# Optimization experiments

Hardware: AMD Instinct MI355X
Metric: run time of the kernel (lower is better)

The kernel has to match this reference:

```python
import jax, jax.numpy as jnp
import numpy as np

D_MODEL = 1024
HEADS = 16
D_K = D_MODEL // HEADS


def setup_inputs() -> dict:
    key = jax.random.key(0)
    ks = jax.random.split(key, 12)
    B, S = 2, 2048
    scale = 1.0 / np.sqrt(D_MODEL)
    inp = {
        "q": jax.random.normal(ks[0], (B, S, D_MODEL), dtype=jnp.float32),
        "k": jax.random.normal(ks[1], (B, S, D_MODEL), dtype=jnp.float32),
        "v": jax.random.normal(ks[2], (B, S, D_MODEL), dtype=jnp.float32),
        "src_mask": jax.random.randint(ks[3], (B, 1, S), 0, 2, dtype=jnp.int32),
        # projection params (nn.Linear: y = x @ W.T + b); store W already transposed
        "Wq": jax.random.normal(ks[4], (D_MODEL, D_MODEL), dtype=jnp.float32) * scale,
        "bq": jnp.zeros((D_MODEL,), dtype=jnp.float32),
        "Wk": jax.random.normal(ks[5], (D_MODEL, D_MODEL), dtype=jnp.float32) * scale,
        "bk": jnp.zeros((D_MODEL,), dtype=jnp.float32),
        "Wv": jax.random.normal(ks[6], (D_MODEL, D_MODEL), dtype=jnp.float32) * scale,
        "bv": jnp.zeros((D_MODEL,), dtype=jnp.float32),
        "Wo": jax.random.normal(ks[7], (D_MODEL, D_MODEL), dtype=jnp.float32) * scale,
        "bo": jnp.zeros((D_MODEL,), dtype=jnp.float32),
    }
    return inp


def reference(q, k, v, src_mask, Wq, bq, Wk, bk, Wv, bv, Wo, bo):
    B, S, _ = q.shape
    # QKV projections, reshape to (b, heads, seq, d_k)
    def proj(x, W, b):
        y = x @ W + b  # (b, s, d_model)
        return y.reshape(B, S, HEADS, D_K).transpose(0, 2, 1, 3)

    qh = proj(q, Wq, bq)
    kh = proj(k, Wk, bk)
    vh = proj(v, Wv, bv)

    # scaled dot-product attention with padding mask
    scores = jnp.einsum("bhqd,bhkd->bhqk", qh, kh) / jnp.sqrt(jnp.float32(D_K))
    mask = src_mask[:, None, :, :]  # (b,1,1,s), broadcast over heads & query
    scores = jnp.where(mask == 0, jnp.float32(-1e9), scores)
    probs = jax.nn.softmax(scores, axis=-1)
    # dropout is identity in eval mode (reference baseline)
    ctx = jnp.einsum("bhqk,bhkd->bhqd", probs, vh)
    ctx = ctx.transpose(0, 2, 1, 3).reshape(B, S, D_MODEL)
    return ctx @ Wo + bo
```

## Files before the change

### kernel.cpp

```cpp
#include <hip/hip_runtime.h>
#include <hip/hip_bf16.h>

#define DM 1024
#define SL 2048
#define NH 16
#define DK 64

typedef __bf16 bf16;
typedef __bf16 bf16x8 __attribute__((ext_vector_type(8)));
typedef __bf16 bf16x4 __attribute__((ext_vector_type(4)));
typedef float f32x4 __attribute__((ext_vector_type(4)));
typedef float f32x16 __attribute__((ext_vector_type(16)));
typedef unsigned u32x4 __attribute__((ext_vector_type(4)));

__device__ __forceinline__ void gll16(const void* g, void* l) {
  __builtin_amdgcn_global_load_lds(
      (const __attribute__((address_space(1))) unsigned int*)g,
      (__attribute__((address_space(3))) unsigned int*)l, 16, 0, 0);
}

__device__ __forceinline__ unsigned pk2(float a, float b) {
  unsigned short lo = __builtin_bit_cast(unsigned short, (bf16)a);
  unsigned short hi = __builtin_bit_cast(unsigned short, (bf16)b);
  return (unsigned)lo | ((unsigned)hi << 16);
}

__global__ __launch_bounds__(256) void cvt_x_kernel(
    const float* __restrict__ q, const float* __restrict__ k, const float* __restrict__ v,
    bf16* __restrict__ xq, bf16* __restrict__ xk, bf16* __restrict__ xv) {
  const float* src; bf16* dst;
  if (blockIdx.y == 0)      { src = q; dst = xq; }
  else if (blockIdx.y == 1) { src = k; dst = xk; }
  else                      { src = v; dst = xv; }
  int i = (blockIdx.x * 256 + threadIdx.x) * 8;
  f32x4 a = *(const f32x4*)(src + i);
  f32x4 b = *(const f32x4*)(src + i + 4);
  bf16x8 o;
  o[0]=(bf16)a[0]; o[1]=(bf16)a[1]; o[2]=(bf16)a[2]; o[3]=(bf16)a[3];
  o[4]=(bf16)b[0]; o[5]=(bf16)b[1]; o[6]=(bf16)b[2]; o[7]=(bf16)b[3];
  *(bf16x8*)(dst + i) = o;
}

__global__ __launch_bounds__(256) void cvt_w_kernel(
    const float* __restrict__ W0, const float* __restrict__ W1,
    const float* __restrict__ W2, const float* __restrict__ W3,
    bf16* __restrict__ T0, bf16* __restrict__ T1,
    bf16* __restrict__ T2, bf16* __restrict__ T3) {
  const float* W; bf16* T;
  switch (blockIdx.y) {
    case 0:  W = W0; T = T0; break;
    case 1:  W = W1; T = T1; break;
    case 2:  W = W2; T = T2; break;
    default: W = W3; T = T3; break;
  }
  __shared__ float t[64][65];
  const int tid = threadIdx.x;
  const int tx = blockIdx.x & 15, ty = blockIdx.x >> 4;
  const int cr = tid >> 4, cc = tid & 15;
  #pragma unroll
  for (int rr = 0; rr < 4; ++rr) {
    int row = rr*16 + cr;
    f32x4 val = *(const f32x4*)(W + (ty*64 + row)*DM + tx*64 + cc*4);
    t[row][cc*4+0] = val[0]; t[row][cc*4+1] = val[1];
    t[row][cc*4+2] = val[2]; t[row][cc*4+3] = val[3];
  }
  __syncthreads();
  #pragma unroll
  for (int rr = 0; rr < 4; ++rr) {
    int nrow = rr*16 + cr;
    bf16x4 o;
    o[0] = (bf16)t[cc*4+0][nrow]; o[1] = (bf16)t[cc*4+1][nrow];
    o[2] = (bf16)t[cc*4+2][nrow]; o[3] = (bf16)t[cc*4+3][nrow];
    *(bf16x4*)(T + (tx*64 + nrow)*DM + ty*64 + cc*4) = o;
  }
}

__global__ __launch_bounds__(256) void maskcvt_kernel(
    const int* __restrict__ msk, float* __restrict__ mBias) {
  int i = (blockIdx.x * 256 + threadIdx.x) * 4;
  int4 m4 = *(const int4*)(msk + i);
  f32x4 o;
  o[0] = (m4.x == 0) ? -1.4426950e9f : 0.f;
  o[1] = (m4.y == 0) ? -1.4426950e9f : 0.f;
  o[2] = (m4.z == 0) ? -1.4426950e9f : 0.f;
  o[3] = (m4.w == 0) ? -1.4426950e9f : 0.f;
  *(f32x4*)(mBias + i) = o;
}

template<int MODE>
__device__ __forceinline__ void gemm_core(
    const bf16* __restrict__ A, const bf16* __restrict__ Bt, const float* __restrict__ bias,
    bf16* __restrict__ outH, float* __restrict__ outF) {
  const int bid = blockIdx.x;
  const int swz = (bid & 7) * 64 + (bid >> 3);
  const int mt = swz >> 3, nt = swz & 7;
  const int m0 = mt*64, n0 = nt*128;
  __shared__ __attribute__((aligned(16))) bf16 As[64*64];
  __shared__ __attribute__((aligned(16))) bf16 Bs[128*64];
  const int tid = threadIdx.x, lane = tid & 63, w = tid >> 6;
  const int wm = w >> 1, wn = w & 1;
  f32x4 acc[2][4];
  #pragma unroll
  for (int x = 0; x < 2; ++x)
    #pragma unroll
    for (int y = 0; y < 4; ++y)
      #pragma unroll
      for (int e = 0; e < 4; ++e) acc[x][y][e] = 0.f;

  for (int kt = 0; kt < 16; ++kt) {
    const int k0 = kt*64;
    __syncthreads();
    #pragma unroll
    for (int i = 0; i < 2; ++i) {
      int idx = (i*4 + w)*64 + lane;
      int r = idx >> 3;
      int s = (idx & 7) ^ (r & 7);
      gll16(A + (m0 + r)*DM + k0 + s*8, &As[(i*4 + w)*512]);
    }
    #pragma unroll
    for (int i = 0; i < 4; ++i) {
      int idx = (i*4 + w)*64 + lane;
      int r = idx >> 3;
      int s = (idx & 7) ^ (r & 7);
      gll16(Bt + (n0 + r)*DM + k0 + s*8, &Bs[(i*4 + w)*512]);
    }
    __syncthreads();
    bf16x8 bfr[4][2];
    #pragma unroll
    for (int ni = 0; ni < 4; ++ni) {
      int row = wn*64 + ni*16 + (lane & 15);
      #pragma unroll
      for (int c = 0; c < 2; ++c) {
        int slot = (lane >> 4) + c*4;
        bfr[ni][c] = *(const bf16x8*)&Bs[row*64 + ((slot ^ (row & 7)) << 3)];
      }
    }
    __builtin_amdgcn_s_setprio(1);
    #pragma unroll
    for (int mi = 0; mi < 2; ++mi) {
      int row = wm*32 + mi*16 + (lane & 15);
      bf16x8 a0 = *(const bf16x8*)&As[row*64 + ((((lane >> 4)    ) ^ (row & 7)) << 3)];
      bf16x8 a1 = *(const bf16x8*)&As[row*64 + ((((lane >> 4) + 4) ^ (row & 7)) << 3)];
      #pragma unroll
      for (int ni = 0; ni < 4; ++ni) {
        acc[mi][ni] = __builtin_amdgcn_mfma_f32_16x16x32_bf16(a0, bfr[ni][0], acc[mi][ni], 0, 0, 0);
        acc[mi][ni] = __builtin_amdgcn_mfma_f32_16x16x32_bf16(a1, bfr[ni][1], acc[mi][ni], 0, 0, 0);
      }
    }
    __builtin_amdgcn_s_setprio(0);
  }
  #pragma unroll
  for (int ni = 0; ni < 4; ++ni) {
    int n = n0 + wn*64 + ni*16 + (lane & 15);
    float bv = bias[n];
    #pragma unroll
    for (int mi = 0; mi < 2; ++mi) {
      int mb = m0 + wm*32 + mi*16 + ((lane >> 4) << 2);
      if (MODE == 2) {
        int bb = mb >> 11, ss = mb & 2047, hh = n >> 6, dd = n & 63;
        bf16x4 o;
        #pragma unroll
        for (int j = 0; j < 4; ++j) o[j] = (bf16)(acc[mi][ni][j] + bv);
        *(bf16x4*)&outH[(((bb << 4) + hh)*DK + dd)*SL + ss] = o;
      } else {
        #pragma unroll
        for (int j = 0; j < 4; ++j) {
          int m = mb + j;
          float val = acc[mi][ni][j] + bv;
          if (MODE == 1) {
            int bb = m >> 11, ss = m & 2047, hh = n >> 6, dd = n & 63;
            outH[(((bb << 4) + hh)*SL + ss)*DK + dd] = (bf16)val;
          } else {
            outF[m*DM + n] = val;
          }
        }
      }
    }
  }
}

__global__ __launch_bounds__(256, 4) void proj_gemm_kernel(
    const bf16* XQ, const bf16* XK, const bf16* XV,
    const bf16* WTQp, const bf16* WTKp, const bf16* WTVp,
    const float* bq, const float* bk, const float* bv,
    bf16* QHp, bf16* KHp, bf16* VTp) {
  if (blockIdx.y == 0)      gemm_core<1>(XQ, WTQp, bq, QHp, nullptr);
  else if (blockIdx.y == 1) gemm_core<1>(XK, WTKp, bk, KHp, nullptr);
  else                      gemm_core<2>(XV, WTVp, bv, VTp, nullptr);
}

__global__ __launch_bounds__(256, 4) void out_gemm_kernel(
    const bf16* CTXp, const bf16* WTOp, const float* bo, float* out) {
  gemm_core<0>(CTXp, WTOp, bo, nullptr, out);
}

__global__ __launch_bounds__(256, 2) void attn_kernel(
    const bf16* __restrict__ QHp, const bf16* __restrict__ KHp,
    const bf16* __restrict__ VTp, const float* __restrict__ mBias,
    bf16* __restrict__ CTXp) {
  const int d = blockIdx.x;
  const int xcd = d & 7, rr = d >> 3;
  const int bh = xcd*4 + (rr >> 4);
  const int qt = rr & 15;
  const int b = bh >> 4, h = bh & 15;
  const int q0 = qt * 128;
  const bf16* Qp  = QHp + bh * SL * DK;
  const bf16* Kp  = KHp + bh * SL * DK;
  const bf16* Vtp = VTp + bh * SL * DK;
  const float* mb_ = mBias + b * SL;
  __shared__ __attribute__((aligned(16))) bf16 Ks[2][64*64];
  __shared__ __attribute__((aligned(16))) bf16 Vts[2][64*64];
  const int tid = threadIdx.x, lane = tid & 63, w = tid >> 6;
  const int hi = lane >> 5, l5 = lane & 31;
  const float SCL2E = 0.18033688f;

  bf16x8 qf[4];
  {
    const bf16* qr = Qp + (q0 + w*32 + l5)*DK + hi*8;
    #pragma unroll
    for (int c = 0; c < 4; ++c) qf[c] = *(const bf16x8*)(qr + c*16);
  }
  f32x16 o0, o1;
  #pragma unroll
  for (int e = 0; e < 16; ++e) { o0[e] = 0.f; o1[e] = 0.f; }
  float m_run = -1e30f, l_run = 0.f;

  #define STAGE(buf, kt_)                                                  \
    {                                                                      \
      const int k0s = (kt_)*64;                                            \
      _Pragma("unroll")                                                    \
      for (int i = 0; i < 2; ++i) {                                        \
        int idx = (i*4 + w)*64 + lane;                                     \
        int r = idx >> 3;                                                  \
        int s = (idx & 7) ^ (r & 7);                                       \
        gll16(Kp + (k0s + r)*DK + s*8, &Ks[buf][(i*4 + w)*512]);           \
      }                                                                    \
      _Pragma("unroll")                                                    \
      for (int i = 0; i < 2; ++i) {                                        \
        int idx = (i*4 + w)*64 + lane;                                     \
        int r = idx >> 3;                                                  \
        int s = (idx & 7) ^ (r & 7);                                       \
        gll16(Vtp + r*SL + k0s + s*8, &Vts[buf][(i*4 + w)*512]);           \
      }                                                                    \
    }

  STAGE(0, 0);
  __syncthreads();

  for (int kt = 0; kt < 32; ++kt) {
    const int cur = kt & 1;
    const int k0 = kt*64;

    f32x4 mreg[2][4];
    #pragma unroll
    for (int half = 0; half < 2; ++half)
      #pragma unroll
      for (int qd = 0; qd < 4; ++qd)
        mreg[half][qd] = *(const f32x4*)&mb_[k0 + half*32 + qd*8 + hi*4];

    if (kt < 31) STAGE(cur ^ 1, kt + 1);

    f32x16 s0, s1;
    #pragma unroll
    for (int e = 0; e < 16; ++e) { s0[e] = 0.f; s1[e] = 0.f; }
    __builtin_amdgcn_s_setprio(1);
    #pragma unroll
    for (int c = 0; c < 4; ++c) {
      int sl = 2*c + hi;
      int r0 = l5, r1 = 32 + l5;
      bf16x8 kf0 = *(const bf16x8*)&Ks[cur][r0*64 + ((sl ^ (r0 & 7)) << 3)];
      bf16x8 kf1 = *(const bf16x8*)&Ks[cur][r1*64 + ((sl ^ (r1 & 7)) << 3)];
      s0 = __builtin_amdgcn_mfma_f32_32x32x16_bf16(kf0, qf[c], s0, 0, 0, 0);
      s1 = __builtin_amdgcn_mfma_f32_32x32x16_bf16(kf1, qf[c], s1, 0, 0, 0);
    }
    __builtin_amdgcn_s_setprio(0);

    float pv_[32];
    float mtv0 = -1e30f, mtv1 = -1e30f, mtv2 = -1e30f, mtv3 = -1e30f;
    #pragma unroll
    for (int half = 0; half < 2; ++half) {
      #pragma unroll
      for (int qd = 0; qd < 4; ++qd) {
        f32x4 ma = mreg[half][qd];
        #pragma unroll
        for (int j = 0; j < 4; ++j) {
          float val = (half ? s1[qd*4+j] : s0[qd*4+j]) * SCL2E + ma[j];
          pv_[half*16 + qd*4 + j] = val;
          if (j == 0) mtv0 = fmaxf(mtv0, val);
          else if (j == 1) mtv1 = fmaxf(mtv1, val);
          else if (j == 2) mtv2 = fmaxf(mtv2, val);
          else mtv3 = fmaxf(mtv3, val);
        }
      }
    }
    float mt = fmaxf(fmaxf(mtv0, mtv1), fmaxf(mtv2, mtv3));
    mt = fmaxf(mt, __shfl_xor(mt, 32));
    if (!__all(mt - m_run <= 11.5f)) {
      float mnew = fmaxf(m_run, mt);
      float sf = exp2f(m_run - mnew);
      #pragma unroll
      for (int reg = 0; reg < 16; ++reg) {
        int crow = (reg & 3) + ((reg >> 2) << 3) + (hi << 2);
        float s_ = __shfl(sf, crow);
        o0[reg] *= s_; o1[reg] *= s_;
      }
      l_run *= sf;
      m_run = mnew;
    }
    float ls0 = 0.f, ls1 = 0.f, ls2 = 0.f, ls3 = 0.f;
    #pragma unroll
    for (int t = 0; t < 32; ++t) {
      float p = exp2f(pv_[t] - m_run);
      pv_[t] = p;
      if ((t & 3) == 0) ls0 += p;
      else if ((t & 3) == 1) ls1 += p;
      else if ((t & 3) == 2) ls2 += p;
      else ls3 += p;
    }
    float lsum = (ls0 + ls1) + (ls2 + ls3);
    lsum += __shfl_xor(lsum, 32);
    l_run += lsum;

    #pragma unroll
    for (int c = 0; c < 4; ++c) {
      const int half_c = c >> 1;
      const int iA = half_c*16 + (((2*c)    ) & 3)*4;
      const int iB = half_c*16 + (((2*c) + 1) & 3)*4;
      unsigned wA0 = pk2(pv_[iA],   pv_[iA+1]);
      unsigned wA1 = pk2(pv_[iA+2], pv_[iA+3]);
      unsigned wB0 = pk2(pv_[iB],   pv_[iB+1]);
      unsigned wB1 = pk2(pv_[iB+2], pv_[iB+3]);
      unsigned ow0 = hi ? wB0 : wA0, ow1 = hi ? wB1 : wA1;
      unsigned xw0 = hi ? wA0 : wB0, xw1 = hi ? wA1 : wB1;
      unsigned yw0 = __shfl_xor(xw0, 32);
      unsigned yw1 = __shfl_xor(xw1, 32);
      u32x4 uu;
      uu[0] = hi ? yw0 : ow0;
      uu[1] = hi ? yw1 : ow1;
      uu[2] = hi ? ow0 : yw0;
      uu[3] = hi ? ow1 : yw1;
      bf16x8 pa = __builtin_bit_cast(bf16x8, uu);
      int sl = 2*c + hi;
      int r0 = l5, r1 = 32 + l5;
      bf16x8 vf0 = *(const bf16x8*)&Vts[cur][r0*64 + ((sl ^ (r0 & 7)) << 3)];
      bf16x8 vf1 = *(const bf16x8*)&Vts[cur][r1*64 + ((sl ^ (r1 & 7)) << 3)];
      __builtin_amdgcn_s_setprio(1);
      o0 = __builtin_amdgcn_mfma_f32_32x32x16_bf16(pa, vf0, o0, 0, 0, 0);
      o1 = __builtin_amdgcn_mfma_f32_32x32x16_bf16(pa, vf1, o1, 0, 0, 0);
      __builtin_amdgcn_s_setprio(0);
    }
    __syncthreads();
  }

  float inv = 1.f / l_run;
  const int sbase = (b * SL) * DM + h * DK;
  #pragma unroll
  for (int reg = 0; reg < 16; ++reg) {
    int crow = (reg & 3) + ((reg >> 2) << 3) + (hi << 2);
    float iv = __shfl(inv, crow);
    int srow = q0 + w*32 + crow;
    CTXp[sbase + srow*DM + l5]      = (bf16)(o0[reg] * iv);
    CTXp[sbase + srow*DM + 32 + l5] = (bf16)(o1[reg] * iv);
  }
  #undef STAGE
}

extern "C" void kernel_launch(void* const* d_in, const int* in_sizes, int n_in,
                              void* d_out, int out_size, void* d_ws, size_t ws_size,
                              hipStream_t stream) {
  const float* q  = (const float*)d_in[0];
  const float* k  = (const float*)d_in[1];
  const float* v  = (const float*)d_in[2];
  const int*  msk = (const int*)d_in[3];
  const float* Wq = (const float*)d_in[4];
  const float* bq = (const float*)d_in[5];
  const float* Wk = (const float*)d_in[6];
  const float* bk = (const float*)d_in[7];
  const float* Wv = (const float*)d_in[8];
  const float* bv = (const float*)d_in[9];
  const float* Wo = (const float*)d_in[10];
  const float* bo = (const float*)d_in[11];
  char* ws = (char*)d_ws;
  bf16* XQ  = (bf16*)(ws + 0);
  bf16* XK  = (bf16*)(ws + 8388608);
  bf16* XV  = (bf16*)(ws + 16777216);
  bf16* WTQ = (bf16*)(ws + 25165824);
  bf16* WTK = (bf16*)(ws + 27262976);
  bf16* WTV = (bf16*)(ws + 29360128);
  bf16* WTO = (bf16*)(ws + 31457280);
  bf16* QHb = (bf16*)(ws + 33554432);
  bf16* KHb = (bf16*)(ws + 41943040);
  bf16* VTb = (bf16*)(ws + 50331648);
  bf16* CTX = (bf16*)(ws + 58720256);
  float* mBias = (float*)(ws + 0);
  float* out = (float*)d_out;

  cvt_x_kernel<<<dim3(2048, 3), 256, 0, stream>>>(q, k, v, XQ, XK, XV);
  cvt_w_kernel<<<dim3(256, 4), 256, 0, stream>>>(Wq, Wk, Wv, Wo, WTQ, WTK, WTV, WTO);
  proj_gemm_kernel<<<dim3(512, 3), 256, 0, stream>>>(XQ, XK, XV, WTQ, WTK, WTV,
                                                     bq, bk, bv, QHb, KHb, VTb);
  maskcvt_kernel<<<dim3(4), 256, 0, stream>>>(msk, mBias);
  attn_kernel<<<dim3(512), 256, 0, stream>>>(QHb, KHb, VTb, mBias, CTX);
  out_gemm_kernel<<<dim3(512), 256, 0, stream>>>(CTX, WTO, bo, out);
}
```

Before: 258.4 us.

## Double-buffer GEMM tiles, merge conversion kernels, fold mask conversion into attention

The projection and output GEMMs now double-buffer their A/B tiles in LDS. The next k-tile's global-to-LDS load is issued before computing on the current one, with one barrier per iteration instead of two. The input and weight conversion kernels become a single launch, and the mask-bias kernel is dropped: attention now reads the int mask directly and converts it inline. This cuts two launches and overlaps load latency with MFMA work. The cost is doubled GEMM LDS usage, which forces the launch-bounds occupancy hint down from 4 to 3, plus a few extra selects per attention tile.

```diff
diff --git a/kernel.cpp b/kernel.cpp
--- a/kernel.cpp
+++ b/kernel.cpp
@@ -25,66 +25,56 @@
   return (unsigned)lo | ((unsigned)hi << 16);
 }
 
-__global__ __launch_bounds__(256) void cvt_x_kernel(
+__global__ __launch_bounds__(256) void prep_kernel(
     const float* __restrict__ q, const float* __restrict__ k, const float* __restrict__ v,
-    bf16* __restrict__ xq, bf16* __restrict__ xk, bf16* __restrict__ xv) {
-  const float* src; bf16* dst;
-  if (blockIdx.y == 0)      { src = q; dst = xq; }
-  else if (blockIdx.y == 1) { src = k; dst = xk; }
-  else                      { src = v; dst = xv; }
-  int i = (blockIdx.x * 256 + threadIdx.x) * 8;
-  f32x4 a = *(const f32x4*)(src + i);
-  f32x4 b = *(const f32x4*)(src + i + 4);
-  bf16x8 o;
-  o[0]=(bf16)a[0]; o[1]=(bf16)a[1]; o[2]=(bf16)a[2]; o[3]=(bf16)a[3];
-  o[4]=(bf16)b[0]; o[5]=(bf16)b[1]; o[6]=(bf16)b[2]; o[7]=(bf16)b[3];
-  *(bf16x8*)(dst + i) = o;
-}
-
-__global__ __launch_bounds__(256) void cvt_w_kernel(
-    const float* __restrict__ W0, const float* __restrict__ W1,
-    const float* __restrict__ W2, const float* __restrict__ W3,
-    bf16* __restrict__ T0, bf16* __restrict__ T1,
-    bf16* __restrict__ T2, bf16* __restrict__ T3) {
-  const float* W; bf16* T;
-  switch (blockIdx.y) {
-    case 0:  W = W0; T = T0; break;
-    case 1:  W = W1; T = T1; break;
-    case 2:  W = W2; T = T2; break;
-    default: W = W3; T = T3; break;
-  }
+    const float* __restrict__ Wq, const float* __restrict__ Wk,
+    const float* __restrict__ Wv, const float* __restrict__ Wo,
+    bf16* __restrict__ xq, bf16* __restrict__ xk, bf16* __restrict__ xv,
+    bf16* __restrict__ TQ, bf16* __restrict__ TK, bf16* __restrict__ TV,
+    bf16* __restrict__ TO) {
   __shared__ float t[64][65];
-  const int tid = threadIdx.x;
-  const int tx = blockIdx.x & 15, ty = blockIdx.x >> 4;
-  const int cr = tid >> 4, cc = tid & 15;
-  #pragma unroll
-  for (int rr = 0; rr < 4; ++rr) {
-    int row = rr*16 + cr;
-    f32x4 val = *(const f32x4*)(W + (ty*64 + row)*DM + tx*64 + cc*4);
-    t[row][cc*4+0] = val[0]; t[row][cc*4+1] = val[1];
-    t[row][cc*4+2] = val[2]; t[row][cc*4+3] = val[3];
-  }
-  __syncthreads();
-  #pragma unroll
-  for (int rr = 0; rr < 4; ++rr) {
-    int nrow = rr*16 + cr;
-    bf16x4 o;
-    o[0] = (bf16)t[cc*4+0][nrow]; o[1] = (bf16)t[cc*4+1][nrow];
-    o[2] = (bf16)t[cc*4+2][nrow]; o[3] = (bf16)t[cc*4+3][nrow];
-    *(bf16x4*)(T + (tx*64 + nrow)*DM + ty*64 + cc*4) = o;
-  }
-}
-
-__global__ __launch_bounds__(256) void maskcvt_kernel(
-    const int* __restrict__ msk, float* __restrict__ mBias) {
-  int i = (blockIdx.x * 256 + threadIdx.x) * 4;
-  int4 m4 = *(const int4*)(msk + i);
-  f32x4 o;
-  o[0] = (m4.x == 0) ? -1.4426950e9f : 0.f;
-  o[1] = (m4.y == 0) ? -1.4426950e9f : 0.f;
-  o[2] = (m4.z == 0) ? -1.4426950e9f : 0.f;
-  o[3] = (m4.w == 0) ? -1.4426950e9f : 0.f;
-  *(f32x4*)(mBias + i) = o;
+  const int bid = blockIdx.x, tid = threadIdx.x;
+  if (bid < 6144) {
+    const float* src; bf16* dst;
+    if (bid < 2048)      { src = q; dst = xq; }
+    else if (bid < 4096) { src = k; dst = xk; }
+    else                 { src = v; dst = xv; }
+    int i = (bid & 2047) * 2048 + tid * 8;
+    f32x4 a = *(const f32x4*)(src + i);
+    f32x4 b = *(const f32x4*)(src + i + 4);
+    bf16x8 o;
+    o[0]=(bf16)a[0]; o[1]=(bf16)a[1]; o[2]=(bf16)a[2]; o[3]=(bf16)a[3];
+    o[4]=(bf16)b[0]; o[5]=(bf16)b[1]; o[6]=(bf16)b[2]; o[7]=(bf16)b[3];
+    *(bf16x8*)(dst + i) = o;
+  } else {
+    const int wb = bid - 6144;
+    const float* W; bf16* T;
+    switch (wb >> 8) {
+      case 0:  W = Wq; T = TQ; break;
+      case 1:  W = Wk; T = TK; break;
+      case 2:  W = Wv; T = TV; break;
+      default: W = Wo; T = TO; break;
+    }
+    const int tile = wb & 255;
+    const int tx = tile & 15, ty = tile >> 4;
+    const int cr = tid >> 4, cc = tid & 15;
+    #pragma unroll
+    for (int rr = 0; rr < 4; ++rr) {
+      int row = rr*16 + cr;
+      f32x4 val = *(const f32x4*)(W + (ty*64 + row)*DM + tx*64 + cc*4);
+      t[row][cc*4+0] = val[0]; t[row][cc*4+1] = val[1];
+      t[row][cc*4+2] = val[2]; t[row][cc*4+3] = val[3];
+    }
+    __syncthreads();
+    #pragma unroll
+    for (int rr = 0; rr < 4; ++rr) {
+      int nrow = rr*16 + cr;
+      bf16x4 o;
+      o[0] = (bf16)t[cc*4+0][nrow]; o[1] = (bf16)t[cc*4+1][nrow];
+      o[2] = (bf16)t[cc*4+2][nrow]; o[3] = (bf16)t[cc*4+3][nrow];
+      *(bf16x4*)(T + (tx*64 + nrow)*DM + ty*64 + cc*4) = o;
+    }
+  }
 }
 
 template<int MODE>
@@ -95,8 +85,8 @@
   const int swz = (bid & 7) * 64 + (bid >> 3);
   const int mt = swz >> 3, nt = swz & 7;
   const int m0 = mt*64, n0 = nt*128;
-  __shared__ __attribute__((aligned(16))) bf16 As[64*64];
-  __shared__ __attribute__((aligned(16))) bf16 Bs[128*64];
+  __shared__ __attribute__((aligned(16))) bf16 As[2][64*64];
+  __shared__ __attribute__((aligned(16))) bf16 Bs[2][128*64];
   const int tid = threadIdx.x, lane = tid & 63, w = tid >> 6;
   const int wm = w >> 1, wn = w & 1;
   f32x4 acc[2][4];
@@ -107,24 +97,31 @@
       #pragma unroll
       for (int e = 0; e < 4; ++e) acc[x][y][e] = 0.f;
 
+  #define GSTAGE(buf, kt_)                                                 \
+    {                                                                      \
+      const int k0s = (kt_)*64;                                            \
+      _Pragma("unroll")                                                    \
+      for (int i = 0; i < 2; ++i) {                                        \
+        int idx = (i*4 + w)*64 + lane;                                     \
+        int r = idx >> 3;                                                  \
+        int s = (idx & 7) ^ (r & 7);                                       \
+        gll16(A + (m0 + r)*DM + k0s + s*8, &As[buf][(i*4 + w)*512]);       \
+      }                                                                    \
+      _Pragma("unroll")                                                    \
+      for (int i = 0; i < 4; ++i) {                                        \
+        int idx = (i*4 + w)*64 + lane;                                     \
+        int r = idx >> 3;                                                  \
+        int s = (idx & 7) ^ (r & 7);                                       \
+        gll16(Bt + (n0 + r)*DM + k0s + s*8, &Bs[buf][(i*4 + w)*512]);      \
+      }                                                                    \
+    }
+
+  GSTAGE(0, 0);
+  __syncthreads();
+
   for (int kt = 0; kt < 16; ++kt) {
-    const int k0 = kt*64;
-    __syncthreads();
-    #pragma unroll
-    for (int i = 0; i < 2; ++i) {
-      int idx = (i*4 + w)*64 + lane;
-      int r = idx >> 3;
-      int s = (idx & 7) ^ (r & 7);
-      gll16(A + (m0 + r)*DM + k0 + s*8, &As[(i*4 + w)*512]);
-    }
-    #pragma unroll
-    for (int i = 0; i < 4; ++i) {
-      int idx = (i*4 + w)*64 + lane;
-      int r = idx >> 3;
-      int s = (idx & 7) ^ (r & 7);
-      gll16(Bt + (n0 + r)*DM + k0 + s*8, &Bs[(i*4 + w)*512]);
-    }
-    __syncthreads();
+    const int cur = kt & 1;
+    if (kt < 15) GSTAGE(cur ^ 1, kt + 1);
     bf16x8 bfr[4][2];
     #pragma unroll
     for (int ni = 0; ni < 4; ++ni) {
@@ -132,15 +129,15 @@
       #pragma unroll
       for (int c = 0; c < 2; ++c) {
         int slot = (lane >> 4) + c*4;
-        bfr[ni][c] = *(const bf16x8*)&Bs[row*64 + ((slot ^ (row & 7)) << 3)];
+        bfr[ni][c] = *(const bf16x8*)&Bs[cur][row*64 + ((slot ^ (row & 7)) << 3)];
       }
     }
     __builtin_amdgcn_s_setprio(1);
     #pragma unroll
     for (int mi = 0; mi < 2; ++mi) {
       int row = wm*32 + mi*16 + (lane & 15);
-      bf16x8 a0 = *(const bf16x8*)&As[row*64 + ((((lane >> 4)    ) ^ (row & 7)) << 3)];
-      bf16x8 a1 = *(const bf16x8*)&As[row*64 + ((((lane >> 4) + 4) ^ (row & 7)) << 3)];
+      bf16x8 a0 = *(const bf16x8*)&As[cur][row*64 + ((((lane >> 4)    ) ^ (row & 7)) << 3)];
+      bf16x8 a1 = *(const bf16x8*)&As[cur][row*64 + ((((lane >> 4) + 4) ^ (row & 7)) << 3)];
       #pragma unroll
       for (int ni = 0; ni < 4; ++ni) {
         acc[mi][ni] = __builtin_amdgcn_mfma_f32_16x16x32_bf16(a0, bfr[ni][0], acc[mi][ni], 0, 0, 0);
@@ -148,7 +145,10 @@
       }
     }
     __builtin_amdgcn_s_setprio(0);
-  }
+    __syncthreads();
+  }
+  #undef GSTAGE
+
   #pragma unroll
   for (int ni = 0; ni < 4; ++ni) {
     int n = n0 + wn*64 + ni*16 + (lane & 15);
@@ -179,7 +179,7 @@
   }
 }
 
-__global__ __launch_bounds__(256, 4) void proj_gemm_kernel(
+__global__ __launch_bounds__(256, 3) void proj_gemm_kernel(
     const bf16* XQ, const bf16* XK, const bf16* XV,
     const bf16* WTQp, const bf16* WTKp, const bf16* WTVp,
     const float* bq, const float* bk, const float* bv,
@@ -189,14 +189,14 @@
   else                      gemm_core<2>(XV, WTVp, bv, VTp, nullptr);
 }
 
-__global__ __launch_bounds__(256, 4) void out_gemm_kernel(
+__global__ __launch_bounds__(256, 3) void out_gemm_kernel(
     const bf16* CTXp, const bf16* WTOp, const float* bo, float* out) {
   gemm_core<0>(CTXp, WTOp, bo, nullptr, out);
 }
 
 __global__ __launch_bounds__(256, 2) void attn_kernel(
     const bf16* __restrict__ QHp, const bf16* __restrict__ KHp,
-    const bf16* __restrict__ VTp, const float* __restrict__ mBias,
+    const bf16* __restrict__ VTp, const int* __restrict__ msk,
     bf16* __restrict__ CTXp) {
   const int d = blockIdx.x;
   const int xcd = d & 7, rr = d >> 3;
@@ -207,7 +207,7 @@
   const bf16* Qp  = QHp + bh * SL * DK;
   const bf16* Kp  = KHp + bh * SL * DK;
   const bf16* Vtp = VTp + bh * SL * DK;
-  const float* mb_ = mBias + b * SL;
+  const int* mp = msk + b * SL;
   __shared__ __attribute__((aligned(16))) bf16 Ks[2][64*64];
   __shared__ __attribute__((aligned(16))) bf16 Vts[2][64*64];
   const int tid = threadIdx.x, lane = tid & 63, w = tid >> 6;
@@ -255,8 +255,13 @@
     #pragma unroll
     for (int half = 0; half < 2; ++half)
       #pragma unroll
-      for (int qd = 0; qd < 4; ++qd)
-        mreg[half][qd] = *(const f32x4*)&mb_[k0 + half*32 + qd*8 + hi*4];
+      for (int qd = 0; qd < 4; ++qd) {
+        int4 m4 = *(const int4*)&mp[k0 + half*32 + qd*8 + hi*4];
+        mreg[half][qd][0] = m4.x ? 0.f : -1.4426950e9f;
+        mreg[half][qd][1] = m4.y ? 0.f : -1.4426950e9f;
+        mreg[half][qd][2] = m4.z ? 0.f : -1.4426950e9f;
+        mreg[half][qd][3] = m4.w ? 0.f : -1.4426950e9f;
+      }
 
     if (kt < 31) STAGE(cur ^ 1, kt + 1);
 
@@ -392,14 +397,12 @@
   bf16* KHb = (bf16*)(ws + 41943040);
   bf16* VTb = (bf16*)(ws + 50331648);
   bf16* CTX = (bf16*)(ws + 58720256);
-  float* mBias = (float*)(ws + 0);
   float* out = (float*)d_out;
 
-  cvt_x_kernel<<<dim3(2048, 3), 256, 0, stream>>>(q, k, v, XQ, XK, XV);
-  cvt_w_kernel<<<dim3(256, 4), 256, 0, stream>>>(Wq, Wk, Wv, Wo, WTQ, WTK, WTV, WTO);
+  prep_kernel<<<dim3(7168), 256, 0, stream>>>(q, k, v, Wq, Wk, Wv, Wo,
+                                              XQ, XK, XV, WTQ, WTK, WTV, WTO);
   proj_gemm_kernel<<<dim3(512, 3), 256, 0, stream>>>(XQ, XK, XV, WTQ, WTK, WTV,
                                                      bq, bk, bv, QHb, KHb, VTb);
-  maskcvt_kernel<<<dim3(4), 256, 0, stream>>>(msk, mBias);
-  attn_kernel<<<dim3(512), 256, 0, stream>>>(QHb, KHb, VTb, mBias, CTX);
+  attn_kernel<<<dim3(512), 256, 0, stream>>>(QHb, KHb, VTb, msk, CTX);
   out_gemm_kernel<<<dim3(512), 256, 0, stream>>>(CTX, WTO, bo, out);
 }
```

Result: slower. 310.0 us (+20.0%).
